# Optimization experiments

Measured on AMD Instinct MI355X. Metric: run time of the kernel, lower is better.

## Reference

```python
import jax, jax.numpy as jnp
import numpy as np
from jax import lax

BS = 131072
L = 128          # pitch dim (conv input length)
NUM_CH = 10
EMB = 256
Z_DIM = 128
K = 64           # num codebook embeddings
COMMIT = 0.25


def setup_inputs() -> dict:
    key = jax.random.key(0)
    ks = jax.random.split(key, 10)
    pr = jax.random.uniform(ks[0], (BS, L), dtype=jnp.float32)
    track_pad_mask = jax.random.randint(ks[1], (BS,), 0, 2).astype(jnp.bool_)
    conv_w = jax.random.normal(ks[2], (NUM_CH, 1, 12), dtype=jnp.float32) * 0.1
    conv_b = jnp.zeros((NUM_CH,), jnp.float32)
    fc_w = jax.random.normal(ks[3], (EMB, NUM_CH * 29), dtype=jnp.float32) * 0.05
    fc_b = jnp.zeros((EMB,), jnp.float32)
    mu_w = jax.random.normal(ks[4], (Z_DIM, EMB), dtype=jnp.float32) * 0.05
    mu_b = jnp.zeros((Z_DIM,), jnp.float32)
    codebook = jax.random.normal(ks[5], (K, Z_DIM), dtype=jnp.float32)
    return {"pr": pr, "track_pad_mask": track_pad_mask, "conv_w": conv_w,
            "conv_b": conv_b, "fc_w": fc_w, "fc_b": fc_b,
            "mu_w": mu_w, "mu_b": mu_b, "codebook": codebook}


def _encode(pr, conv_w, conv_b, fc_w, fc_b, mu_w, mu_b):
    # Conv1d(1 -> NUM_CH, k=12, stride=1, VALID): [bs,1,128] -> [bs,10,117]
    x = lax.conv_general_dilated(pr[:, None, :], conv_w, (1,), 'VALID',
                                 dimension_numbers=('NCH', 'OIH', 'NCH'))
    x = jax.nn.relu(x + conv_b[None, :, None])
    # MaxPool1d(4,4): [bs,10,117] -> [bs,10,29]
    x = lax.reduce_window(x, -jnp.inf, lax.max, (1, 1, 4), (1, 1, 4), 'VALID')
    x = x.reshape(x.shape[0], -1)               # [bs, 290]
    x = x @ fc_w.T + fc_b                       # [bs, 256]
    mu = x @ mu_w.T + mu_b                      # [bs, 128]
    return mu


def _vq(mu, codebook, track_pad_mask):
    # squared L2 distances [bs, K]
    d = (jnp.sum(mu * mu, axis=1, keepdims=True)
         - 2.0 * mu @ codebook.T
         + jnp.sum(codebook * codebook, axis=1)[None, :])
    idx = jnp.argmin(d, axis=1)                 # [bs]
    q = codebook[idx]                           # gather [bs, Z_DIM]
    valid = (~track_pad_mask).astype(mu.dtype)  # [bs]
    n_valid = jnp.maximum(jnp.sum(valid), 1.0)
    # commitment loss over non-padded rows
    e_latent = jnp.sum(((lax.stop_gradient(q) - mu) ** 2) * valid[:, None]) / (n_valid * mu.shape[1])
    cmt_loss = COMMIT * e_latent
    # straight-through estimator
    z = mu + lax.stop_gradient(q - mu)
    # perplexity over non-padded assignments
    counts = jnp.zeros((K,), mu.dtype).at[idx].add(valid)
    probs = counts / n_valid
    perplexity = jnp.exp(-jnp.sum(probs * jnp.log(probs + 1e-10)))
    return z, cmt_loss, perplexity


def reference(pr, track_pad_mask, conv_w, conv_b, fc_w, fc_b, mu_w, mu_b, codebook):
    mu = _encode(pr, conv_w, conv_b, fc_w, fc_b, mu_w, mu_b)
    z, cmt_loss, perplexity = _vq(mu, codebook, track_pad_mask)
    return z, cmt_loss, perplexity
```

## Files before the change

### kernel.cpp

```cpp
#include <hip/hip_runtime.h>
#include <math.h>

#define BS 131072
#define L 128
#define NCH 10
#define EMB 256
#define ZD 128
#define KCB 64
#define NF 290
#define RPB 64
#define TPB 128

#define MUP 132

typedef __attribute__((ext_vector_type(8))) short short8;
typedef __attribute__((ext_vector_type(4))) float float4v;

#define WS_BC    0
#define WS_CNORM 128
#define WS_CBT   192
#define WS_CNT   8384
#define WS_ESUM  8448
#define WS_WHI   8452
#define WS_WLO   28932

static __device__ __forceinline__ short f2bf(float x) {
  unsigned u = __float_as_uint(x);
  return (short)((u + 0x7fffu + ((u >> 16) & 1u)) >> 16);
}
static __device__ __forceinline__ float bf2f(short s) {
  return __uint_as_float(((unsigned)(unsigned short)s) << 16);
}

__global__ void k_prep(const float* __restrict__ fc_w, const float* __restrict__ fc_b,
                       const float* __restrict__ mu_w, const float* __restrict__ mu_b,
                       const float* __restrict__ codebook, float* __restrict__ ws) {
  const int b = blockIdx.x, t = threadIdx.x;
  if (b < 80) {
    __shared__ float fcT[32 * 260];
    __shared__ float mus[16 * 260];
    const int c = b >> 4, ks = (b >> 3) & 1, nt = b & 7;
    const int f0 = c * 58 + ks * 32;

    {
      const int kk = t & 31, esub = t >> 5;
      const bool valid = (ks * 32 + kk) < 58;
#pragma unroll
      for (int p = 0; p < 32; ++p) {
        int e = p * 8 + esub;
        fcT[kk * 260 + e] = valid ? fc_w[e * NF + f0 + kk] : 0.0f;
      }
    }
    {
#pragma unroll
      for (int p = 0; p < 4; ++p) {
        int idx = p * 256 + t;
        int zz = idx >> 6, e4 = idx & 63;
        *(float4*)&mus[zz * 260 + e4 * 4] =
            *(const float4*)&mu_w[(nt * 16 + zz) * EMB + e4 * 4];
      }
    }
    __syncthreads();

    const int lane_lo = t >> 3, j = t & 7;
    const int z = lane_lo & 15;
    const int kka = ((lane_lo >> 4) & 1) * 8 + j;
    const int kkb = kka + 16;
    float a0 = 0, a1 = 0, a2 = 0, a3 = 0, b0 = 0, b1 = 0, b2 = 0, b3 = 0;
#pragma unroll 8
    for (int e = 0; e < 256; e += 4) {
      float4 m  = *(const float4*)&mus[z * 260 + e];
      float4 fa = *(const float4*)&fcT[kka * 260 + e];
      float4 fb = *(const float4*)&fcT[kkb * 260 + e];
      a0 = fmaf(m.x, fa.x, a0); a1 = fmaf(m.y, fa.y, a1);
      a2 = fmaf(m.z, fa.z, a2); a3 = fmaf(m.w, fa.w, a3);
      b0 = fmaf(m.x, fb.x, b0); b1 = fmaf(m.y, fb.y, b1);
      b2 = fmaf(m.z, fb.z, b2); b3 = fmaf(m.w, fb.w, b3);
    }
    float va = (a0 + a1) + (a2 + a3);
    float vb = (b0 + b1) + (b2 + b3);
    short* hi = (short*)(ws + WS_WHI);
    short* lo = (short*)(ws + WS_WLO);
    const int base = b * 512;
    short ha = f2bf(va); short la = f2bf(va - bf2f(ha));
    short hb = f2bf(vb); short lb = f2bf(vb - bf2f(hb));
    hi[base + t] = ha;        lo[base + t] = la;
    hi[base + 256 + t] = hb;  lo[base + 256 + t] = lb;
  } else if (b == 80) {
    if (t < ZD) {
      float p0 = 0, p1 = 0, p2 = 0, p3 = 0;
      const float* mw = mu_w + (size_t)t * EMB;
      for (int e = 0; e < EMB; e += 4) {
        p0 = fmaf(mw[e + 0], fc_b[e + 0], p0);
        p1 = fmaf(mw[e + 1], fc_b[e + 1], p1);
        p2 = fmaf(mw[e + 2], fc_b[e + 2], p2);
        p3 = fmaf(mw[e + 3], fc_b[e + 3], p3);
      }
      ws[WS_BC + t] = mu_b[t] + ((p0 + p1) + (p2 + p3));
    }
  } else if (b == 81) {
    if (t < KCB) {
      double acc = 0.0;
      for (int k = 0; k < ZD; ++k) { double v = (double)codebook[t * ZD + k]; acc += v * v; }
      ws[WS_CNORM + t] = (float)acc;
    } else if (t < 128) {
      ((int*)ws)[WS_CNT + (t - 64)] = 0;
    } else if (t == 128) {
      ws[WS_ESUM] = 0.0f;
    }
  } else {
    for (int i = 0; i < 32; ++i) {
      int idx = i * 256 + t;
      int k = idx >> 6, cc = idx & 63;
      ws[WS_CBT + idx] = codebook[cc * ZD + k];
    }
  }
}

__launch_bounds__(TPB, 2)
__global__ void k_main(const float* __restrict__ pr, const int* __restrict__ mask,
                       const float* __restrict__ conv_w, const float* __restrict__ conv_b,
                       const float* __restrict__ codebook,
                       float* __restrict__ ws, float* __restrict__ out) {
  __shared__ __align__(16) unsigned char lds_raw[33792];
  __shared__ float aux_val[RPB * 8];
  __shared__ int   aux_idx[RPB * 8];
  __shared__ int   bi_s[RPB];
  __shared__ float validf[RPB];
  __shared__ int   hist[KCB];

  short* feat_hi = (short*)lds_raw;
  short* feat_lo = (short*)(lds_raw + 9216);
  float* mu_s    = (float*)lds_raw;

  const int tid = threadIdx.x;
  const int lane = tid & 63, wv = tid >> 6;
  const int q4 = lane >> 4, c16 = lane & 15;
  const long rowg0 = (long)blockIdx.x * RPB;

  if (tid < KCB) hist[tid] = 0;
  for (int i = tid; i < RPB * 6; i += TPB) {
    int r = i / 6, kk = 58 + (i % 6);
    feat_hi[r * 72 + kk] = 0;
    feat_lo[r * 72 + kk] = 0;
  }

  const float* bc = ws + WS_BC;
  float4v acc[4][4];
#pragma unroll
  for (int ntl = 0; ntl < 4; ++ntl) {
    float bv = bc[wv * 64 + ntl * 16 + c16];
    float4v b4 = {bv, bv, bv, bv};
#pragma unroll
    for (int mt = 0; mt < 4; ++mt) acc[mt][ntl] = b4;
  }

  const short* whi = (const short*)(ws + WS_WHI);
  const short* wlo = (const short*)(ws + WS_WLO);

  const int cr = tid >> 1, hh = tid & 1;
  const float* prow = pr + (rowg0 + cr) * (long)L;
  const int j0 = hh * 15, njj = 15 - hh;

  const float4 wbi0 = *(const float4*)&prow[4 * j0];
  const float4 wbi1 = *(const float4*)&prow[4 * j0 + 4];
  const float4 wbi2 = *(const float4*)&prow[4 * j0 + 8];
  const float4 wbi3 = *(const float4*)&prow[4 * j0 + 12];

#pragma unroll 1
  for (int ck = 0; ck < 5; ++ck) {
    short8 pbh[4], pbl[4];
#pragma unroll
    for (int ntl = 0; ntl < 4; ++ntl) {
      int nt = wv * 4 + ntl;
      int fo = (((ck * 2 + 0) * 8 + nt) * 64 + lane) * 8;
      pbh[ntl] = *(const short8*)(whi + fo);
      pbl[ntl] = *(const short8*)(wlo + fo);
    }

    {
      const int ch0 = ck * 2;
      float w0[12], w1[12];
#pragma unroll
      for (int u = 0; u < 12; ++u) {
        w0[u] = conv_w[ch0 * 12 + u];
        w1[u] = conv_w[ch0 * 12 + 12 + u];
      }
      const float cb0 = conv_b[ch0], cb1 = conv_b[ch0 + 1];

      float wb[20];
      *(float4*)&wb[0]  = wbi0;
      *(float4*)&wb[4]  = wbi1;
      *(float4*)&wb[8]  = wbi2;
      *(float4*)&wb[12] = wbi3;
#pragma unroll
      for (int jj = 0; jj < 15; ++jj) {
        if (jj < njj) {
          int j = j0 + jj;
          if (jj + 1 < njj)
            *(float4*)&wb[((jj + 4) % 5) * 4] = *(const float4*)&prow[4 * j + 16];
          float m40 = -1e30f, m41 = -1e30f;
#pragma unroll
          for (int d = 0; d < 4; ++d) {
            float a0 = cb0, a1 = cb1;
#pragma unroll
            for (int u = 0; u < 12; ++u) {
              float x = wb[(4 * jj + d + u) % 20];
              a0 = fmaf(w0[u], x, a0);
              a1 = fmaf(w1[u], x, a1);
            }
            m40 = fmaxf(m40, a0);
            m41 = fmaxf(m41, a1);
          }
          float v0 = fmaxf(m40, 0.0f);
          float v1 = fmaxf(m41, 0.0f);
          short h0 = f2bf(v0);
          feat_hi[cr * 72 + j] = h0;
          feat_lo[cr * 72 + j] = f2bf(v0 - bf2f(h0));
          short h1 = f2bf(v1);
          feat_hi[cr * 72 + 29 + j] = h1;
          feat_lo[cr * 72 + 29 + j] = f2bf(v1 - bf2f(h1));
        }
      }
    }
    __syncthreads();

    {
      short8 ah[4], al[4];
#pragma unroll
      for (int mt = 0; mt < 4; ++mt) {
        int off = (mt * 16 + c16) * 72 + q4 * 8;
        ah[mt] = *(const short8*)(feat_hi + off);
        al[mt] = *(const short8*)(feat_lo + off);
      }
#pragma unroll
      for (int ntl = 0; ntl < 4; ++ntl) {
#pragma unroll
        for (int mt = 0; mt < 4; ++mt) {
          acc[mt][ntl] = __builtin_amdgcn_mfma_f32_16x16x32_bf16(ah[mt], pbh[ntl], acc[mt][ntl], 0, 0, 0);
          acc[mt][ntl] = __builtin_amdgcn_mfma_f32_16x16x32_bf16(ah[mt], pbl[ntl], acc[mt][ntl], 0, 0, 0);
          acc[mt][ntl] = __builtin_amdgcn_mfma_f32_16x16x32_bf16(al[mt], pbh[ntl], acc[mt][ntl], 0, 0, 0);
        }
      }
    }
    {
      short8 ah[4], al[4];
#pragma unroll
      for (int mt = 0; mt < 4; ++mt) {
        int off = (mt * 16 + c16) * 72 + 32 + q4 * 8;
        ah[mt] = *(const short8*)(feat_hi + off);
        al[mt] = *(const short8*)(feat_lo + off);
      }
#pragma unroll
      for (int ntl = 0; ntl < 4; ++ntl) {
        int nt = wv * 4 + ntl;
        int fo = (((ck * 2 + 1) * 8 + nt) * 64 + lane) * 8;
        short8 bh = *(const short8*)(whi + fo);
        short8 bl = *(const short8*)(wlo + fo);
#pragma unroll
        for (int mt = 0; mt < 4; ++mt) {
          acc[mt][ntl] = __builtin_amdgcn_mfma_f32_16x16x32_bf16(ah[mt], bh, acc[mt][ntl], 0, 0, 0);
          acc[mt][ntl] = __builtin_amdgcn_mfma_f32_16x16x32_bf16(ah[mt], bl, acc[mt][ntl], 0, 0, 0);
          acc[mt][ntl] = __builtin_amdgcn_mfma_f32_16x16x32_bf16(al[mt], bh, acc[mt][ntl], 0, 0, 0);
        }
      }
    }
    __syncthreads();
  }

#pragma unroll
  for (int mt = 0; mt < 4; ++mt)
#pragma unroll
    for (int ntl = 0; ntl < 4; ++ntl) {
      int col = wv * 64 + ntl * 16 + c16;
      int rowb = mt * 16 + q4 * 4;
#pragma unroll
      for (int r = 0; r < 4; ++r)
        mu_s[(rowb + r) * MUP + col] = acc[mt][ntl][r];
    }
  __syncthreads();

  const float* cnorm = ws + WS_CNORM;
  const float* cbT   = ws + WS_CBT;
  const int tvr = tid & 15, tvc = tid >> 4;
  const int rv0 = tvr * 4, cbo = tvc * 8;
  float s[4][8];
#pragma unroll
  for (int i = 0; i < 4; ++i)
#pragma unroll
    for (int j = 0; j < 8; ++j) s[i][j] = 0.0f;
#pragma unroll 2
  for (int k4 = 0; k4 < 128; k4 += 4) {
    float4 mr0 = *(const float4*)&mu_s[(rv0 + 0) * MUP + k4];
    float4 mr1 = *(const float4*)&mu_s[(rv0 + 1) * MUP + k4];
    float4 mr2 = *(const float4*)&mu_s[(rv0 + 2) * MUP + k4];
    float4 mr3 = *(const float4*)&mu_s[(rv0 + 3) * MUP + k4];
#pragma unroll
    for (int kk = 0; kk < 4; ++kk) {
      int k = k4 + kk;
      float4 ca = *(const float4*)&cbT[k * 64 + cbo];
      float4 cb4 = *(const float4*)&cbT[k * 64 + cbo + 4];
      float cv[8] = {ca.x, ca.y, ca.z, ca.w, cb4.x, cb4.y, cb4.z, cb4.w};
      float mv[4] = {((const float*)&mr0)[kk], ((const float*)&mr1)[kk],
                     ((const float*)&mr2)[kk], ((const float*)&mr3)[kk]};
#pragma unroll
      for (int i = 0; i < 4; ++i)
#pragma unroll
        for (int j = 0; j < 8; ++j) s[i][j] = fmaf(mv[i], cv[j], s[i][j]);
    }
  }
  {
    float4 n0 = *(const float4*)&cnorm[cbo];
    float4 n1 = *(const float4*)&cnorm[cbo + 4];
    float nv[8] = {n0.x, n0.y, n0.z, n0.w, n1.x, n1.y, n1.z, n1.w};
#pragma unroll
    for (int i = 0; i < 4; ++i) {
      float best = nv[0] - 2.0f * s[i][0];
      int bi = cbo;
#pragma unroll
      for (int j = 1; j < 8; ++j) {
        float d = nv[j] - 2.0f * s[i][j];
        if (d < best) { best = d; bi = cbo + j; }
      }
      aux_val[(rv0 + i) * 8 + tvc] = best;
      aux_idx[(rv0 + i) * 8 + tvc] = bi;
    }
  }
  __syncthreads();

  if (tid < RPB) {
    float best = aux_val[tid * 8];
    int bi = aux_idx[tid * 8];
#pragma unroll
    for (int v = 1; v < 8; ++v) {
      float x = aux_val[tid * 8 + v];
      if (x < best) { best = x; bi = aux_idx[tid * 8 + v]; }
    }
    bi_s[tid] = bi;
    validf[tid] = (mask[rowg0 + tid] == 0) ? 1.0f : 0.0f;
  }
  __syncthreads();
  if (tid < RPB) {
    if (validf[tid] > 0.5f) atomicAdd(&hist[bi_s[tid]], 1);
  }
  __syncthreads();
  if (tid < KCB && hist[tid] > 0) atomicAdd(&((int*)ws)[WS_CNT + tid], hist[tid]);

  float eloc = 0.0f;
  float* zout = out + rowg0 * ZD;
#pragma unroll 8
  for (int p = 0; p < RPB; ++p) {
    int bi = bi_s[p];
    float q = codebook[bi * ZD + tid];
    float m = mu_s[p * MUP + tid];
    zout[(size_t)p * ZD + tid] = q;
    float d = q - m;
    eloc += validf[p] * d * d;
  }
#pragma unroll
  for (int o = 32; o > 0; o >>= 1) eloc += __shfl_xor(eloc, o, 64);
  if ((tid & 63) == 0) atomicAdd(&ws[WS_ESUM], eloc);
}

__global__ void k_final(const float* __restrict__ ws, float* __restrict__ out) {
  int t = threadIdx.x;
  const int* cnt = (const int*)ws + WS_CNT;
  double c = (double)cnt[t];
  double nv = c;
#pragma unroll
  for (int o = 32; o > 0; o >>= 1) nv += __shfl_xor(nv, o, 64);
  nv = fmax(nv, 1.0);
  double p = c / nv;
  double h = p * log(p + 1e-10);
#pragma unroll
  for (int o = 32; o > 0; o >>= 1) h += __shfl_xor(h, o, 64);
  if (t == 0) {
    out[(size_t)BS * ZD]     = (float)(0.25 * (double)ws[WS_ESUM] / (nv * 128.0));
    out[(size_t)BS * ZD + 1] = (float)exp(-h);
  }
}

extern "C" void kernel_launch(void* const* d_in, const int* in_sizes, int n_in,
                              void* d_out, int out_size, void* d_ws, size_t ws_size,
                              hipStream_t stream) {
  const float* pr      = (const float*)d_in[0];
  const int*   mask    = (const int*)d_in[1];
  const float* conv_w  = (const float*)d_in[2];
  const float* conv_b  = (const float*)d_in[3];
  const float* fc_w    = (const float*)d_in[4];
  const float* fc_b    = (const float*)d_in[5];
  const float* mu_w    = (const float*)d_in[6];
  const float* mu_b    = (const float*)d_in[7];
  const float* codebook= (const float*)d_in[8];
  float* ws  = (float*)d_ws;
  float* out = (float*)d_out;

  hipLaunchKernelGGL(k_prep, dim3(83), dim3(256), 0, stream,
                     fc_w, fc_b, mu_w, mu_b, codebook, ws);
  hipLaunchKernelGGL(k_main, dim3(BS / RPB), dim3(TPB), 0, stream,
                     pr, mask, conv_w, conv_b, codebook, ws, out);
  hipLaunchKernelGGL(k_final, dim3(1), dim3(64), 0, stream, ws, out);
}
```

Measured before the change: 301.6 us.

## Fold codebook distance into MFMA GEMM via precomputed Wf·codebook weights

Precomputes the fused feature-to-codebook score matrix (fc_w·mu_w composed with the codebook) in a new prep kernel. The main kernel then gets codebook dot products straight from extra bf16 MFMA tiles on the features, instead of running a separate fp32 FMA distance loop over mu. Block size doubles to 256 threads, and the conv work is split across 4 threads per row. The argmin now uses a shuffle reduction with index tie-breaking. The risk is that distances come from the composed weights in split-bf16 precision, which may flip near-tie argmins compared with the reference; an out-buffer scratch region is also used for the intermediate weights.

```diff
diff --git a/kernel.cpp b/kernel.cpp
--- a/kernel.cpp
+++ b/kernel.cpp
@@ -9,20 +9,17 @@
 #define KCB 64
 #define NF 290
 #define RPB 64
-#define TPB 128
-
-#define MUP 132
+#define TPB 256
 
 typedef __attribute__((ext_vector_type(8))) short short8;
 typedef __attribute__((ext_vector_type(4))) float float4v;
 
 #define WS_BC    0
-#define WS_CNORM 128
-#define WS_CBT   192
-#define WS_CNT   8384
-#define WS_ESUM  8448
-#define WS_WHI   8452
-#define WS_WLO   28932
+#define WS_DPART 128
+#define WS_CNT   192
+#define WS_ESUM  256
+#define WS_WHI   260
+#define WS_WLO   30980
 
 static __device__ __forceinline__ short f2bf(float x) {
   unsigned u = __float_as_uint(x);
@@ -34,12 +31,14 @@
 
 __global__ void k_prep(const float* __restrict__ fc_w, const float* __restrict__ fc_b,
                        const float* __restrict__ mu_w, const float* __restrict__ mu_b,
-                       const float* __restrict__ codebook, float* __restrict__ ws) {
+                       const float* __restrict__ codebook, float* __restrict__ ws,
+                       float* __restrict__ wf) {
   const int b = blockIdx.x, t = threadIdx.x;
   if (b < 80) {
     __shared__ float fcT[32 * 260];
     __shared__ float mus[16 * 260];
     const int c = b >> 4, ks = (b >> 3) & 1, nt = b & 7;
+    const int g = c * 2 + ks;
     const int f0 = c * 58 + ks * 32;
 
     {
@@ -81,11 +80,14 @@
     float vb = (b0 + b1) + (b2 + b3);
     short* hi = (short*)(ws + WS_WHI);
     short* lo = (short*)(ws + WS_WLO);
-    const int base = b * 512;
+    const int base = (g * 12 + nt) * 512;
     short ha = f2bf(va); short la = f2bf(va - bf2f(ha));
     short hb = f2bf(vb); short lb = f2bf(vb - bf2f(hb));
     hi[base + t] = ha;        lo[base + t] = la;
     hi[base + 256 + t] = hb;  lo[base + 256 + t] = lb;
+    const int zg = nt * 16 + z;
+    if (ks * 32 + kka < 58) wf[(f0 + kka) * 128 + zg] = va;
+    if (ks * 32 + kkb < 58) wf[(f0 + kkb) * 128 + zg] = vb;
   } else if (b == 80) {
     if (t < ZD) {
       float p0 = 0, p1 = 0, p2 = 0, p3 = 0;
@@ -98,21 +100,56 @@
       }
       ws[WS_BC + t] = mu_b[t] + ((p0 + p1) + (p2 + p3));
     }
-  } else if (b == 81) {
+  } else {
+    if (t < KCB) ((int*)ws)[WS_CNT + t] = 0;
+    else if (t == KCB) ws[WS_ESUM] = 0.0f;
+  }
+}
+
+__global__ void k_prep2(const float* __restrict__ codebook, const float* __restrict__ wf,
+                        float* __restrict__ ws) {
+  const int b = blockIdx.x, t = threadIdx.x;
+  if (b < 40) {
+    const int g = b >> 2, nt_s = b & 3;
+    const int ck = g >> 1, ksb = g & 1;
+    short* hi = (short*)(ws + WS_WHI);
+    short* lo = (short*)(ws + WS_WLO);
+    const int base = (g * 12 + 8 + nt_s) * 512;
+#pragma unroll
+    for (int half = 0; half < 2; ++half) {
+      const int idx = half * 256 + t;
+      const int lane = idx >> 3, j = idx & 7;
+      const int klq = ksb * 32 + (lane >> 4) * 8 + j;
+      const int c = nt_s * 16 + (lane & 15);
+      short h = 0, l = 0;
+      if (klq < 58) {
+        const int f = ck * 58 + klq;
+        const float* wfr = wf + (size_t)f * 128;
+        const float* cbr = codebook + (size_t)c * ZD;
+        float p0 = 0, p1 = 0, p2 = 0, p3 = 0;
+#pragma unroll 8
+        for (int z = 0; z < 128; z += 4) {
+          float4 a  = *(const float4*)&wfr[z];
+          float4 cv = *(const float4*)&cbr[z];
+          p0 = fmaf(a.x, cv.x, p0); p1 = fmaf(a.y, cv.y, p1);
+          p2 = fmaf(a.z, cv.z, p2); p3 = fmaf(a.w, cv.w, p3);
+        }
+        float v = (p0 + p1) + (p2 + p3);
+        h = f2bf(v);
+        l = f2bf(v - bf2f(h));
+      }
+      hi[base + idx] = h;
+      lo[base + idx] = l;
+    }
+  } else {
     if (t < KCB) {
-      double acc = 0.0;
-      for (int k = 0; k < ZD; ++k) { double v = (double)codebook[t * ZD + k]; acc += v * v; }
-      ws[WS_CNORM + t] = (float)acc;
-    } else if (t < 128) {
-      ((int*)ws)[WS_CNT + (t - 64)] = 0;
-    } else if (t == 128) {
-      ws[WS_ESUM] = 0.0f;
-    }
-  } else {
-    for (int i = 0; i < 32; ++i) {
-      int idx = i * 256 + t;
-      int k = idx >> 6, cc = idx & 63;
-      ws[WS_CBT + idx] = codebook[cc * ZD + k];
+      double cn = 0.0, bs = 0.0;
+      for (int z = 0; z < 128; ++z) {
+        double cv = (double)codebook[t * ZD + z];
+        cn += cv * cv;
+        bs += (double)ws[WS_BC + z] * cv;
+      }
+      ws[WS_DPART + t] = (float)(cn - 2.0 * bs);
     }
   }
 }
@@ -122,9 +159,9 @@
                        const float* __restrict__ conv_w, const float* __restrict__ conv_b,
                        const float* __restrict__ codebook,
                        float* __restrict__ ws, float* __restrict__ out) {
-  __shared__ __align__(16) unsigned char lds_raw[33792];
-  __shared__ float aux_val[RPB * 8];
-  __shared__ int   aux_idx[RPB * 8];
+  __shared__ __align__(16) unsigned char lds_raw[33024];
+  __shared__ float aux_val[RPB * 4];
+  __shared__ int   aux_idx[RPB * 4];
   __shared__ int   bi_s[RPB];
   __shared__ float validf[RPB];
   __shared__ int   hist[KCB];
@@ -134,7 +171,7 @@
   float* mu_s    = (float*)lds_raw;
 
   const int tid = threadIdx.x;
-  const int lane = tid & 63, wv = tid >> 6;
+  const int lane = tid & 63, w = tid >> 6;
   const int q4 = lane >> 4, c16 = lane & 15;
   const long rowg0 = (long)blockIdx.x * RPB;
 
@@ -146,21 +183,25 @@
   }
 
   const float* bc = ws + WS_BC;
-  float4v acc[4][4];
-#pragma unroll
-  for (int ntl = 0; ntl < 4; ++ntl) {
-    float bv = bc[wv * 64 + ntl * 16 + c16];
+  float4v accm[4][2];
+  float4v accs[4];
+#pragma unroll
+  for (int ntl = 0; ntl < 2; ++ntl) {
+    float bv = bc[w * 32 + ntl * 16 + c16];
     float4v b4 = {bv, bv, bv, bv};
 #pragma unroll
-    for (int mt = 0; mt < 4; ++mt) acc[mt][ntl] = b4;
-  }
+    for (int mt = 0; mt < 4; ++mt) accm[mt][ntl] = b4;
+  }
+#pragma unroll
+  for (int mt = 0; mt < 4; ++mt) accs[mt] = (float4v){0.f, 0.f, 0.f, 0.f};
 
   const short* whi = (const short*)(ws + WS_WHI);
   const short* wlo = (const short*)(ws + WS_WLO);
 
-  const int cr = tid >> 1, hh = tid & 1;
+  const int cr = tid >> 2, qq = tid & 3;
   const float* prow = pr + (rowg0 + cr) * (long)L;
-  const int j0 = hh * 15, njj = 15 - hh;
+  const int j0 = qq ? (7 * qq + 1) : 0;
+  const int njj = qq ? 7 : 8;
 
   const float4 wbi0 = *(const float4*)&prow[4 * j0];
   const float4 wbi1 = *(const float4*)&prow[4 * j0 + 4];
@@ -169,15 +210,6 @@
 
 #pragma unroll 1
   for (int ck = 0; ck < 5; ++ck) {
-    short8 pbh[4], pbl[4];
-#pragma unroll
-    for (int ntl = 0; ntl < 4; ++ntl) {
-      int nt = wv * 4 + ntl;
-      int fo = (((ck * 2 + 0) * 8 + nt) * 64 + lane) * 8;
-      pbh[ntl] = *(const short8*)(whi + fo);
-      pbl[ntl] = *(const short8*)(wlo + fo);
-    }
-
     {
       const int ch0 = ck * 2;
       float w0[12], w1[12];
@@ -194,7 +226,7 @@
       *(float4*)&wb[8]  = wbi2;
       *(float4*)&wb[12] = wbi3;
 #pragma unroll
-      for (int jj = 0; jj < 15; ++jj) {
+      for (int jj = 0; jj < 8; ++jj) {
         if (jj < njj) {
           int j = j0 + jj;
           if (jj + 1 < njj)
@@ -225,43 +257,39 @@
     }
     __syncthreads();
 
-    {
+#pragma unroll
+    for (int ks = 0; ks < 2; ++ks) {
+      const int g = ck * 2 + ks;
       short8 ah[4], al[4];
 #pragma unroll
       for (int mt = 0; mt < 4; ++mt) {
-        int off = (mt * 16 + c16) * 72 + q4 * 8;
+        int off = (mt * 16 + c16) * 72 + ks * 32 + q4 * 8;
         ah[mt] = *(const short8*)(feat_hi + off);
         al[mt] = *(const short8*)(feat_lo + off);
       }
 #pragma unroll
-      for (int ntl = 0; ntl < 4; ++ntl) {
-#pragma unroll
-        for (int mt = 0; mt < 4; ++mt) {
-          acc[mt][ntl] = __builtin_amdgcn_mfma_f32_16x16x32_bf16(ah[mt], pbh[ntl], acc[mt][ntl], 0, 0, 0);
-          acc[mt][ntl] = __builtin_amdgcn_mfma_f32_16x16x32_bf16(ah[mt], pbl[ntl], acc[mt][ntl], 0, 0, 0);
-          acc[mt][ntl] = __builtin_amdgcn_mfma_f32_16x16x32_bf16(al[mt], pbh[ntl], acc[mt][ntl], 0, 0, 0);
-        }
-      }
-    }
-    {
-      short8 ah[4], al[4];
-#pragma unroll
-      for (int mt = 0; mt < 4; ++mt) {
-        int off = (mt * 16 + c16) * 72 + 32 + q4 * 8;
-        ah[mt] = *(const short8*)(feat_hi + off);
-        al[mt] = *(const short8*)(feat_lo + off);
-      }
-#pragma unroll
-      for (int ntl = 0; ntl < 4; ++ntl) {
-        int nt = wv * 4 + ntl;
-        int fo = (((ck * 2 + 1) * 8 + nt) * 64 + lane) * 8;
+      for (int ntl = 0; ntl < 2; ++ntl) {
+        int nt = w * 2 + ntl;
+        int fo = ((g * 12 + nt) * 64 + lane) * 8;
         short8 bh = *(const short8*)(whi + fo);
         short8 bl = *(const short8*)(wlo + fo);
 #pragma unroll
         for (int mt = 0; mt < 4; ++mt) {
-          acc[mt][ntl] = __builtin_amdgcn_mfma_f32_16x16x32_bf16(ah[mt], bh, acc[mt][ntl], 0, 0, 0);
-          acc[mt][ntl] = __builtin_amdgcn_mfma_f32_16x16x32_bf16(ah[mt], bl, acc[mt][ntl], 0, 0, 0);
-          acc[mt][ntl] = __builtin_amdgcn_mfma_f32_16x16x32_bf16(al[mt], bh, acc[mt][ntl], 0, 0, 0);
+          accm[mt][ntl] = __builtin_amdgcn_mfma_f32_16x16x32_bf16(ah[mt], bh, accm[mt][ntl], 0, 0, 0);
+          accm[mt][ntl] = __builtin_amdgcn_mfma_f32_16x16x32_bf16(ah[mt], bl, accm[mt][ntl], 0, 0, 0);
+          accm[mt][ntl] = __builtin_amdgcn_mfma_f32_16x16x32_bf16(al[mt], bh, accm[mt][ntl], 0, 0, 0);
+        }
+      }
+      {
+        int fo = ((g * 12 + 8 + w) * 64 + lane) * 8;
+        short8 sbh = *(const short8*)(whi + fo);
+        short8 sbl = *(const short8*)(wlo + fo);
+#pragma unroll
+        for (int mt = 0; mt < 4; ++mt) {
+          accs[mt] = __builtin_amdgcn_mfma_f32_16x16x32_bf16(ah[mt], sbh, accs[mt], 0, 0, 0);
+          accs[mt] = __builtin_amdgcn_mfma_f32_16x16x32_bf16(ah[mt], sbl, accs[mt], 0, 0, 0);
+          accs[mt] = __builtin_amdgcn_mfma_f32_16x16x32_bf16(al[mt], sbh, accs[mt], 0, 0, 0);
+          accs[mt] = __builtin_amdgcn_mfma_f32_16x16x32_bf16(al[mt], sbl, accs[mt], 0, 0, 0);
         }
       }
     }
@@ -271,89 +299,63 @@
 #pragma unroll
   for (int mt = 0; mt < 4; ++mt)
 #pragma unroll
-    for (int ntl = 0; ntl < 4; ++ntl) {
-      int col = wv * 64 + ntl * 16 + c16;
+    for (int ntl = 0; ntl < 2; ++ntl) {
+      int col = w * 32 + ntl * 16 + c16;
       int rowb = mt * 16 + q4 * 4;
 #pragma unroll
       for (int r = 0; r < 4; ++r)
-        mu_s[(rowb + r) * MUP + col] = acc[mt][ntl][r];
-    }
+        mu_s[(rowb + r) * 129 + col] = accm[mt][ntl][r];
+    }
+
+  {
+    const float dp = ws[WS_DPART + w * 16 + c16];
+#pragma unroll
+    for (int mt = 0; mt < 4; ++mt)
+#pragma unroll
+      for (int r = 0; r < 4; ++r) {
+        float val = fmaf(-2.0f, accs[mt][r], dp);
+        int idx = w * 16 + c16;
+#pragma unroll
+        for (int msk = 1; msk <= 8; msk <<= 1) {
+          float ov = __shfl_xor(val, msk, 64);
+          int   oi = __shfl_xor(idx, msk, 64);
+          if (ov < val || (ov == val && oi < idx)) { val = ov; idx = oi; }
+        }
+        if (c16 == 0) {
+          int row = mt * 16 + q4 * 4 + r;
+          aux_val[row * 4 + w] = val;
+          aux_idx[row * 4 + w] = idx;
+        }
+      }
+  }
   __syncthreads();
 
-  const float* cnorm = ws + WS_CNORM;
-  const float* cbT   = ws + WS_CBT;
-  const int tvr = tid & 15, tvc = tid >> 4;
-  const int rv0 = tvr * 4, cbo = tvc * 8;
-  float s[4][8];
-#pragma unroll
-  for (int i = 0; i < 4; ++i)
-#pragma unroll
-    for (int j = 0; j < 8; ++j) s[i][j] = 0.0f;
-#pragma unroll 2
-  for (int k4 = 0; k4 < 128; k4 += 4) {
-    float4 mr0 = *(const float4*)&mu_s[(rv0 + 0) * MUP + k4];
-    float4 mr1 = *(const float4*)&mu_s[(rv0 + 1) * MUP + k4];
-    float4 mr2 = *(const float4*)&mu_s[(rv0 + 2) * MUP + k4];
-    float4 mr3 = *(const float4*)&mu_s[(rv0 + 3) * MUP + k4];
-#pragma unroll
-    for (int kk = 0; kk < 4; ++kk) {
-      int k = k4 + kk;
-      float4 ca = *(const float4*)&cbT[k * 64 + cbo];
-      float4 cb4 = *(const float4*)&cbT[k * 64 + cbo + 4];
-      float cv[8] = {ca.x, ca.y, ca.z, ca.w, cb4.x, cb4.y, cb4.z, cb4.w};
-      float mv[4] = {((const float*)&mr0)[kk], ((const float*)&mr1)[kk],
-                     ((const float*)&mr2)[kk], ((const float*)&mr3)[kk]};
-#pragma unroll
-      for (int i = 0; i < 4; ++i)
-#pragma unroll
-        for (int j = 0; j < 8; ++j) s[i][j] = fmaf(mv[i], cv[j], s[i][j]);
-    }
-  }
-  {
-    float4 n0 = *(const float4*)&cnorm[cbo];
-    float4 n1 = *(const float4*)&cnorm[cbo + 4];
-    float nv[8] = {n0.x, n0.y, n0.z, n0.w, n1.x, n1.y, n1.z, n1.w};
-#pragma unroll
-    for (int i = 0; i < 4; ++i) {
-      float best = nv[0] - 2.0f * s[i][0];
-      int bi = cbo;
-#pragma unroll
-      for (int j = 1; j < 8; ++j) {
-        float d = nv[j] - 2.0f * s[i][j];
-        if (d < best) { best = d; bi = cbo + j; }
-      }
-      aux_val[(rv0 + i) * 8 + tvc] = best;
-      aux_idx[(rv0 + i) * 8 + tvc] = bi;
-    }
-  }
-  __syncthreads();
-
   if (tid < RPB) {
-    float best = aux_val[tid * 8];
-    int bi = aux_idx[tid * 8];
-#pragma unroll
-    for (int v = 1; v < 8; ++v) {
-      float x = aux_val[tid * 8 + v];
-      if (x < best) { best = x; bi = aux_idx[tid * 8 + v]; }
+    float best = aux_val[tid * 4];
+    int bi = aux_idx[tid * 4];
+#pragma unroll
+    for (int v = 1; v < 4; ++v) {
+      float x = aux_val[tid * 4 + v];
+      int  ii = aux_idx[tid * 4 + v];
+      if (x < best || (x == best && ii < bi)) { best = x; bi = ii; }
     }
     bi_s[tid] = bi;
     validf[tid] = (mask[rowg0 + tid] == 0) ? 1.0f : 0.0f;
   }
   __syncthreads();
-  if (tid < RPB) {
-    if (validf[tid] > 0.5f) atomicAdd(&hist[bi_s[tid]], 1);
-  }
+  if (tid < RPB && validf[tid] > 0.5f) atomicAdd(&hist[bi_s[tid]], 1);
   __syncthreads();
   if (tid < KCB && hist[tid] > 0) atomicAdd(&((int*)ws)[WS_CNT + tid], hist[tid]);
 
+  const int col = tid & 127, phh = tid >> 7;
   float eloc = 0.0f;
   float* zout = out + rowg0 * ZD;
-#pragma unroll 8
-  for (int p = 0; p < RPB; ++p) {
+#pragma unroll 4
+  for (int p = phh; p < RPB; p += 2) {
     int bi = bi_s[p];
-    float q = codebook[bi * ZD + tid];
-    float m = mu_s[p * MUP + tid];
-    zout[(size_t)p * ZD + tid] = q;
+    float q = codebook[bi * ZD + col];
+    float m = mu_s[p * 129 + col];
+    zout[(size_t)p * ZD + col] = q;
     float d = q - m;
     eloc += validf[p] * d * d;
   }
@@ -395,8 +397,10 @@
   float* ws  = (float*)d_ws;
   float* out = (float*)d_out;
 
-  hipLaunchKernelGGL(k_prep, dim3(83), dim3(256), 0, stream,
-                     fc_w, fc_b, mu_w, mu_b, codebook, ws);
+  hipLaunchKernelGGL(k_prep, dim3(82), dim3(256), 0, stream,
+                     fc_w, fc_b, mu_w, mu_b, codebook, ws, out);
+  hipLaunchKernelGGL(k_prep2, dim3(41), dim3(256), 0, stream,
+                     codebook, out, ws);
   hipLaunchKernelGGL(k_main, dim3(BS / RPB), dim3(TPB), 0, stream,
                      pr, mask, conv_w, conv_b, codebook, ws, out);
   hipLaunchKernelGGL(k_final, dim3(1), dim3(64), 0, stream, ws, out);
```

New measurement: 334.4 us. 1.11x slower.
